# Kernel optimization log

Measured on AMD Instinct MI355X. Metric: run time of the kernel, lower is better.

The kernel has to match this reference:

```python
import jax, jax.numpy as jnp
import numpy as np

N = 50000      # nodes
E = 800000     # edges (avg degree 16)
F0 = 3         # node feature dim
EF = 3         # edge feature dim
C = 4          # num classes


def _lin_params(k, din, dout):
    k1, k2 = jax.random.split(k)
    s = 1.0 / np.sqrt(din)
    W = jax.random.uniform(k1, (dout, din), jnp.float32, -s, s)
    b = jax.random.uniform(k2, (dout,), jnp.float32, -s, s)
    return W, b


def setup_inputs() -> dict:
    key = jax.random.key(0)
    ks = jax.random.split(key, 8)
    x = jax.random.normal(ks[0], (N, F0), jnp.float32)
    edge_index = jax.random.randint(ks[1], (2, E), 0, N, jnp.int32)
    edge_attr = jax.random.uniform(ks[2], (E, EF), dtype=jnp.float32)
    W1, b1 = _lin_params(ks[3], 2 * F0 + EF, 128)
    W2, b2 = _lin_params(ks[4], 2 * 128 + EF, 64)
    W3, b3 = _lin_params(ks[5], 2 * 64 + EF, 32)
    Wc, bc = _lin_params(ks[6], 32, C)
    return dict(x=x, edge_index=edge_index, edge_attr=edge_attr,
                W1=W1, b1=b1, W2=W2, b2=b2, W3=W3, b3=b3, Wc=Wc, bc=bc)


def _edgeconv(x, src, dst, ea, W, b, n):
    # message = Linear(cat([x_i, x_j, edge_attr])); aggregated by scatter-add to dst (x_i side).
    # Split W so the node-side matmuls happen once per node instead of per edge.
    f = x.shape[1]
    Wi, Wj, We = W[:, :f], W[:, f:2 * f], W[:, 2 * f:]
    ai = x @ Wi.T   # [N, out]
    aj = x @ Wj.T   # [N, out]
    msg = ai[dst] + aj[src] + ea @ We.T + b  # [E_aug, out]
    return jax.ops.segment_sum(msg, dst, num_segments=n)


def reference(x, edge_index, edge_attr, W1, b1, W2, b2, W3, b3, Wc, bc):
    n = x.shape[0]
    loops = jnp.arange(n, dtype=edge_index.dtype)
    src = jnp.concatenate([edge_index[0], loops])  # x_j indices
    dst = jnp.concatenate([edge_index[1], loops])  # x_i indices (aggregation targets)
    ea = jnp.concatenate([edge_attr, jnp.zeros((n, edge_attr.shape[1]), edge_attr.dtype)])
    h = jax.nn.relu(_edgeconv(x, src, dst, ea, W1, b1, n))
    h = jax.nn.relu(_edgeconv(h, src, dst, ea, W2, b2, n))
    h = _edgeconv(h, src, dst, ea, W3, b3, n)  # no relu after conv3 in the original
    logits = h @ Wc.T + bc
    return jax.nn.log_softmax(logits, axis=1)
```

## Files before the change

kernel.cpp:

```cpp
#include <hip/hip_runtime.h>
#include <math.h>


static inline size_t align256(size_t x) { return (x + 255) & ~size_t(255); }

typedef unsigned short ushort_t;
using frag8  = __attribute__((ext_vector_type(8))) short;
using f32x4v = __attribute__((ext_vector_type(4))) float;
using half8  = __attribute__((ext_vector_type(8))) _Float16;

__device__ inline unsigned short f2bf(float f) {
    unsigned u = __float_as_uint(f);
    unsigned r = (u + 0x7fffu + ((u >> 16) & 1u)) >> 16;
    return (unsigned short)r;
}
__device__ inline float bflo(unsigned u) { return __uint_as_float(u << 16); }
__device__ inline float bfhi(unsigned u) { return __uint_as_float(u & 0xffff0000u); }
__device__ inline ushort_t f2hbits(float f) {
    _Float16 h = (_Float16)f;
    ushort_t u;
    __builtin_memcpy(&u, &h, 2);
    return u;
}


__global__ __launch_bounds__(256) void prep(
    const int* __restrict__ ei, int* __restrict__ count,
    uint2* __restrict__ csrp, const float* __restrict__ ea, int E,
    const float* __restrict__ x, float4* __restrict__ xpad, int n,
    const float* __restrict__ W2, ushort_t* __restrict__ W2bf,
    const float* __restrict__ W3, const float* __restrict__ b3,
    const float* __restrict__ Wc, const float* __restrict__ bc,
    float* __restrict__ AB, float* __restrict__ consts,
    int eb4, int nxb)
{
    const int t = threadIdx.x;
    const int b = blockIdx.x;
    if (b < eb4) {
        int e4 = (b * 256 + t) * 4;
        if (e4 >= E) return;
        if (e4 + 3 < E) {
            int4 s = *(const int4*)(ei + e4);
            int4 d = *(const int4*)(ei + E + e4);
            float4 a = *(const float4*)(ea + (size_t)e4 * 3);
            float4 bq = *(const float4*)(ea + (size_t)e4 * 3 + 4);
            float4 c = *(const float4*)(ea + (size_t)e4 * 3 + 8);
            int4 po;
            po.x = atomicAdd(&count[d.x], 1);
            po.y = atomicAdd(&count[d.y], 1);
            po.z = atomicAdd(&count[d.z], 1);
            po.w = atomicAdd(&count[d.w], 1);
            float ev[12] = { a.x, a.y, a.z, a.w, bq.x, bq.y, bq.z, bq.w, c.x, c.y, c.z, c.w };
            int sv[4] = { s.x, s.y, s.z, s.w };
            int dv[4] = { d.x, d.y, d.z, d.w };
            int pv[4] = { po.x, po.y, po.z, po.w };
            #pragma unroll
            for (int r = 0; r < 4; ++r) {
                uint2 p;
                p.x = (unsigned)f2bf(ev[r * 3 + 0]) | ((unsigned)f2bf(ev[r * 3 + 1]) << 16);
                p.y = (unsigned)f2bf(ev[r * 3 + 2]) | ((unsigned)sv[r] << 16);
                if (pv[r] < 64)
                    csrp[((size_t)dv[r] << 6) + pv[r]] = p;
            }
        } else {
            for (int e = e4; e < E; ++e) {
                int sv = ei[e], dv = ei[E + e];
                int po = atomicAdd(&count[dv], 1);
                uint2 p;
                p.x = (unsigned)f2bf(ea[e * 3 + 0]) | ((unsigned)f2bf(ea[e * 3 + 1]) << 16);
                p.y = (unsigned)f2bf(ea[e * 3 + 2]) | ((unsigned)sv << 16);
                if (po < 64)
                    csrp[((size_t)dv << 6) + po] = p;
            }
        }
    } else if (b < eb4 + nxb) {
        int j = (b - eb4) * 256 + t;
        if (j < n) {
            const float* xp = x + (size_t)j * 3;
            xpad[j] = make_float4(xp[0], xp[1], xp[2], 0.f);
        }
    } else if (b < eb4 + nxb + 4) {
        int wb = b - (eb4 + nxb);
        int i0 = wb * 4096 + t;
        int i1 = (wb + 1) * 4096;
        for (int idx = i0; idx < i1; idx += 256) {
            int jg = idx >> 7, k = idx & 127;
            float w = (jg < 64) ? W2[jg * 259 + k] : W2[(jg - 64) * 259 + 128 + k];
            W2bf[idx] = f2bf(w);
        }
    } else {
        for (int idx = t; idx < 512; idx += 256) {
            int j = idx >> 6, k = idx & 63;
            int jj = j & 3;
            int base = (j >= 4) ? 64 : 0;
            float s = 0.f;
            #pragma unroll
            for (int c = 0; c < 32; ++c)
                s += Wc[jj * 32 + c] * W3[c * 131 + base + k];
            AB[idx] = s;
        }
        if (t < 4) {
            float db = 0.f;
            for (int c = 0; c < 32; ++c) db += Wc[t * 32 + c] * b3[c];
            consts[t] = db;
            consts[4 + t] = bc[t];
            for (int q = 0; q < 3; ++q) {
                float s = 0.f;
                for (int c = 0; c < 32; ++c) s += Wc[t * 32 + c] * W3[c * 131 + 128 + q];
                consts[8 + t * 3 + q] = s;
            }
        }
    }
}


__global__ __launch_bounds__(256) void h1_gemm(
    const float4* __restrict__ xpad, const float* __restrict__ W1,
    const float* __restrict__ b1, const float* __restrict__ b2,
    const int* __restrict__ count,
    const uint2* __restrict__ csrp, float4* __restrict__ eagg4,
    const ushort_t* __restrict__ W2bf,
    _Float16* __restrict__ AI2, _Float16* __restrict__ AJ2, int n_nodes)
{
    constexpr int HS = 152;
    constexpr int OS = 72;
    __shared__ float sM[10 * 128];
    __shared__ ushort_t sH[64 * HS];

    const int tid = threadIdx.x;
    for (int t = tid; t < 1280; t += 256) {
        int k = t >> 7, c = t & 127;
        int cp = (c & 31) * 4 + (c >> 5);
        sM[k * 128 + cp] = (k < 9) ? W1[c * 9 + k] : b1[c];
    }
    __syncthreads();

    const int base = blockIdx.x * 64;

    {
        const int nl = tid >> 2, ch4 = tid & 3;
        const int n = base + nl;
        if (n < n_nodes) {
            int s0 = n << 6;
            int s1 = s0 + count[n];
            float xx = 0.f, xy = 0.f, xz = 0.f, ex = 0.f, ey = 0.f, ez = 0.f;
            int i = s0 + ch4;
            for (; i + 12 < s1; i += 16) {
                uint2 p0 = csrp[i];
                uint2 p1 = csrp[i + 4];
                uint2 p2 = csrp[i + 8];
                uint2 p3 = csrp[i + 12];
                float4 xv0 = xpad[(int)(p0.y >> 16)];
                float4 xv1 = xpad[(int)(p1.y >> 16)];
                float4 xv2 = xpad[(int)(p2.y >> 16)];
                float4 xv3 = xpad[(int)(p3.y >> 16)];
                ex += (bflo(p0.x) + bflo(p1.x)) + (bflo(p2.x) + bflo(p3.x));
                ey += (bfhi(p0.x) + bfhi(p1.x)) + (bfhi(p2.x) + bfhi(p3.x));
                ez += (bflo(p0.y) + bflo(p1.y)) + (bflo(p2.y) + bflo(p3.y));
                xx += (xv0.x + xv1.x) + (xv2.x + xv3.x);
                xy += (xv0.y + xv1.y) + (xv2.y + xv3.y);
                xz += (xv0.z + xv1.z) + (xv2.z + xv3.z);
            }
            for (; i < s1; i += 4) {
                uint2 p0 = csrp[i];
                float4 xv0 = xpad[(int)(p0.y >> 16)];
                ex += bflo(p0.x); ey += bfhi(p0.x); ez += bflo(p0.y);
                xx += xv0.x; xy += xv0.y; xz += xv0.z;
            }
            #pragma unroll
            for (int off = 1; off < 4; off <<= 1) {
                xx += __shfl_xor(xx, off); xy += __shfl_xor(xy, off); xz += __shfl_xor(xz, off);
                ex += __shfl_xor(ex, off); ey += __shfl_xor(ey, off); ez += __shfl_xor(ez, off);
            }
            float deg = (float)(count[n] + 1);
            float4 xs = xpad[n];
            float v[10] = { deg * xs.x, deg * xs.y, deg * xs.z,
                            xs.x + xx, xs.y + xy, xs.z + xz,
                            ex, ey, ez, deg };
            #pragma unroll
            for (int h = 0; h < 2; ++h) {
                float hv[16];
                #pragma unroll
                for (int q = 0; q < 16; ++q) {
                    int cq = h * 16 + q;
                    float s = 0.f;
                    #pragma unroll
                    for (int k = 0; k < 10; ++k) s += v[k] * sM[k * 128 + cq * 4 + ch4];
                    hv[q] = fmaxf(s, 0.f);
                }
                uint4 u0, u1;
                u0.x = (unsigned)f2bf(hv[0]) | ((unsigned)f2bf(hv[1]) << 16);
                u0.y = (unsigned)f2bf(hv[2]) | ((unsigned)f2bf(hv[3]) << 16);
                u0.z = (unsigned)f2bf(hv[4]) | ((unsigned)f2bf(hv[5]) << 16);
                u0.w = (unsigned)f2bf(hv[6]) | ((unsigned)f2bf(hv[7]) << 16);
                u1.x = (unsigned)f2bf(hv[8]) | ((unsigned)f2bf(hv[9]) << 16);
                u1.y = (unsigned)f2bf(hv[10]) | ((unsigned)f2bf(hv[11]) << 16);
                u1.z = (unsigned)f2bf(hv[12]) | ((unsigned)f2bf(hv[13]) << 16);
                u1.w = (unsigned)f2bf(hv[14]) | ((unsigned)f2bf(hv[15]) << 16);
                *(uint4*)(sH + nl * HS + ch4 * 32 + h * 16) = u0;
                *(uint4*)(sH + nl * HS + ch4 * 32 + h * 16 + 8) = u1;
            }
            if (ch4 == 0) eagg4[n] = make_float4(ex, ey, ez, 0.f);
        } else {
            *(uint4*)(sH + nl * HS + ch4 * 32) = make_uint4(0, 0, 0, 0);
            *(uint4*)(sH + nl * HS + ch4 * 32 + 8) = make_uint4(0, 0, 0, 0);
            *(uint4*)(sH + nl * HS + ch4 * 32 + 16) = make_uint4(0, 0, 0, 0);
            *(uint4*)(sH + nl * HS + ch4 * 32 + 24) = make_uint4(0, 0, 0, 0);
        }
    }
    __syncthreads();

    const int wave = tid >> 6, wl = tid & 63;
    const int m = wl & 15, quad = wl >> 4;

    frag8 a[4];
    #pragma unroll
    for (int ks = 0; ks < 4; ++ks)
        a[ks] = *(const frag8*)(sH + (wave * 16 + m) * HS + ks * 32 + quad * 8);

    f32x4v acc[8];
    #pragma unroll
    for (int t = 0; t < 8; ++t) acc[t] = (f32x4v)(0.f);

    #pragma unroll
    for (int t = 0; t < 8; ++t) {
        #pragma unroll
        for (int ks = 0; ks < 4; ++ks) {
            frag8 b = *(const frag8*)(W2bf + (t * 16 + m) * 128 + ks * 32 + quad * 8);
            acc[t] = __builtin_amdgcn_mfma_f32_16x16x32_bf16(a[ks], b, acc[t], 0, 0, 0);
        }
    }

    float b2v[4];
    #pragma unroll
    for (int t = 0; t < 4; ++t) b2v[t] = b2[t * 16 + m];

    __syncthreads();
    ushort_t* sAI = sH;
    ushort_t* sAJ = sH + 64 * OS;

    #pragma unroll
    for (int reg = 0; reg < 4; ++reg) {
        int rl = wave * 16 + quad * 4 + reg;
        #pragma unroll
        for (int t = 0; t < 4; ++t)
            sAI[rl * OS + t * 16 + m] = f2hbits(acc[t][reg] + b2v[t]);
        #pragma unroll
        for (int t = 4; t < 8; ++t)
            sAJ[rl * OS + (t - 4) * 16 + m] = f2hbits(acc[t][reg]);
    }
    __syncthreads();

    for (int idx = tid; idx < 512; idx += 256) {
        int row = idx >> 3, seg = idx & 7;
        int grow = base + row;
        if (grow < n_nodes) {
            *(uint4*)((ushort_t*)AI2 + (size_t)grow * 64 + seg * 8) =
                *(const uint4*)(sAI + row * OS + seg * 8);
            *(uint4*)((ushort_t*)AJ2 + (size_t)grow * 64 + seg * 8) =
                *(const uint4*)(sAJ + row * OS + seg * 8);
        }
    }
}


__global__ __launch_bounds__(256) void gather2(
    const _Float16* __restrict__ AI2, const _Float16* __restrict__ AJ2,
    const float* __restrict__ W2, const int* __restrict__ count,
    const float4* __restrict__ eagg4,
    const uint2* __restrict__ csrp, const float* __restrict__ AB,
    float* __restrict__ U, float* __restrict__ Z, int n_nodes)
{
    __shared__ float sAB[512];
    __shared__ float sWe[192];
    const int tid = threadIdx.x;
    for (int t = tid; t < 512; t += 256) sAB[t] = AB[t];
    for (int t = tid; t < 192; t += 256) {
        int c = t / 3, q = t % 3;
        sWe[t] = W2[c * 259 + 256 + q];
    }
    __syncthreads();

    int wl = tid & 63;
    int grp = wl >> 3, ch8 = wl & 7;
    int n = blockIdx.x * 32 + (tid >> 6) * 8 + grp;
    if (n >= n_nodes) return;

    int s0 = n << 6;
    int s1 = s0 + count[n];

    half8 hacc0 = (half8)(_Float16)0.f;
    half8 hacc1 = (half8)(_Float16)0.f;
    int base = s0;
    for (; base + 8 < s1; base += 16) {
        int jA = base + ch8;
        int jB = base + 8 + ch8; if (jB >= s1) jB = s1 - 1;
        int myA = (int)(csrp[jA].y >> 16);
        int myB = (int)(csrp[jB].y >> 16);
        int cntB = s1 - (base + 8); if (cntB > 8) cntB = 8;
        #pragma unroll
        for (int k = 0; k < 8; ++k) {
            int s = __shfl(myA, grp * 8 + k);
            half8 v = *(const half8*)(AJ2 + (size_t)s * 64 + ch8 * 8);
            if (k & 1) hacc1 += v; else hacc0 += v;
        }
        #pragma unroll
        for (int k = 0; k < 8; ++k) {
            int s = __shfl(myB, grp * 8 + k);
            if (k < cntB) {
                half8 v = *(const half8*)(AJ2 + (size_t)s * 64 + ch8 * 8);
                if (k & 1) hacc1 += v; else hacc0 += v;
            }
        }
    }
    if (base < s1) {
        int j = base + ch8; if (j >= s1) j = s1 - 1;
        int my = (int)(csrp[j].y >> 16);
        int cnt = s1 - base; if (cnt > 8) cnt = 8;
        #pragma unroll
        for (int k = 0; k < 8; ++k) {
            int s = __shfl(my, grp * 8 + k);
            if (k < cnt) {
                half8 v = *(const half8*)(AJ2 + (size_t)s * 64 + ch8 * 8);
                if (k & 1) hacc1 += v; else hacc0 += v;
            }
        }
    }
    float acc[8];
    #pragma unroll
    for (int q = 0; q < 8; ++q) acc[q] = (float)hacc0[q] + (float)hacc1[q];

    float deg = (float)(s1 - s0 + 1);
    float4 e4 = eagg4[n];
    half8 ai = *(const half8*)(AI2 + (size_t)n * 64 + ch8 * 8);
    half8 su = *(const half8*)(AJ2 + (size_t)n * 64 + ch8 * 8);
    float r[8];
    #pragma unroll
    for (int q = 0; q < 8; ++q) {
        int c = ch8 * 8 + q;
        float we = sWe[c * 3] * e4.x + sWe[c * 3 + 1] * e4.y + sWe[c * 3 + 2] * e4.z;
        r[q] = fmaxf(deg * (float)ai[q] + (float)su[q] + we + acc[q], 0.f);
    }
    float pj[8];
    #pragma unroll
    for (int j = 0; j < 8; ++j) {
        float4 wA = *(const float4*)(sAB + j * 64 + ch8 * 8);
        float4 wB = *(const float4*)(sAB + j * 64 + ch8 * 8 + 4);
        pj[j] = r[0] * wA.x + r[1] * wA.y + r[2] * wA.z + r[3] * wA.w
              + r[4] * wB.x + r[5] * wB.y + r[6] * wB.z + r[7] * wB.w;
    }
    #pragma unroll
    for (int off = 1; off < 8; off <<= 1)
        #pragma unroll
        for (int j = 0; j < 8; ++j) pj[j] += __shfl_xor(pj[j], off);

    if (ch8 == 0) {
        *(float4*)(U + (size_t)n * 4) = make_float4(pj[0], pj[1], pj[2], pj[3]);
        *(float4*)(Z + (size_t)n * 4) = make_float4(pj[4], pj[5], pj[6], pj[7]);
    }
}


__global__ __launch_bounds__(256) void final_softmax(
    const float* __restrict__ U, const float* __restrict__ Z,
    const int* __restrict__ count, const float4* __restrict__ eagg4,
    const uint2* __restrict__ csrp, const float* __restrict__ consts,
    float* __restrict__ out, int n_nodes)
{
    int wl = threadIdx.x & 63;
    int grp = wl >> 3, ch8 = wl & 7;
    int n = blockIdx.x * 32 + (threadIdx.x >> 6) * 8 + grp;
    if (n >= n_nodes) return;

    int s0 = n << 6;
    int s1 = s0 + count[n];
    float ax = 0.f, ay = 0.f, az = 0.f, aw = 0.f;
    int i = s0 + ch8;
    for (; i + 8 < s1; i += 16) {
        int sA = (int)(csrp[i].y >> 16);
        int sB = (int)(csrp[i + 8].y >> 16);
        float4 zA = *(const float4*)(Z + (size_t)sA * 4);
        float4 zB = *(const float4*)(Z + (size_t)sB * 4);
        ax += zA.x + zB.x; ay += zA.y + zB.y;
        az += zA.z + zB.z; aw += zA.w + zB.w;
    }
    if (i < s1) {
        int sA = (int)(csrp[i].y >> 16);
        float4 zA = *(const float4*)(Z + (size_t)sA * 4);
        ax += zA.x; ay += zA.y; az += zA.z; aw += zA.w;
    }
    #pragma unroll
    for (int off = 1; off < 8; off <<= 1) {
        ax += __shfl_xor(ax, off); ay += __shfl_xor(ay, off);
        az += __shfl_xor(az, off); aw += __shfl_xor(aw, off);
    }
    if (ch8 != 0) return;

    float deg = (float)(s1 - s0 + 1);
    float4 u = *(const float4*)(U + (size_t)n * 4);
    float4 zs = *(const float4*)(Z + (size_t)n * 4);
    float4 e4 = eagg4[n];
    float av[4] = { ax + zs.x, ay + zs.y, az + zs.z, aw + zs.w };
    float uv[4] = { u.x, u.y, u.z, u.w };
    float lg[4];
    #pragma unroll
    for (int j = 0; j < 4; ++j) {
        lg[j] = deg * (uv[j] + consts[j]) + av[j] + consts[4 + j]
              + consts[8 + j * 3] * e4.x + consts[9 + j * 3] * e4.y
              + consts[10 + j * 3] * e4.z;
    }
    float m = fmaxf(fmaxf(lg[0], lg[1]), fmaxf(lg[2], lg[3]));
    float lse = logf(expf(lg[0] - m) + expf(lg[1] - m) + expf(lg[2] - m) + expf(lg[3] - m));
    *(float4*)(out + (size_t)n * 4) =
        make_float4(lg[0] - m - lse, lg[1] - m - lse, lg[2] - m - lse, lg[3] - m - lse);
}


extern "C" void kernel_launch(void* const* d_in, const int* in_sizes, int n_in,
                              void* d_out, int out_size, void* d_ws, size_t ws_size,
                              hipStream_t stream)
{
    const float* x    = (const float*)d_in[0];
    const int*   ei   = (const int*)  d_in[1];
    const float* ea   = (const float*)d_in[2];
    const float* W1   = (const float*)d_in[3];
    const float* b1   = (const float*)d_in[4];
    const float* W2   = (const float*)d_in[5];
    const float* b2   = (const float*)d_in[6];
    const float* W3   = (const float*)d_in[7];
    const float* b3   = (const float*)d_in[8];
    const float* Wc   = (const float*)d_in[9];
    const float* bc   = (const float*)d_in[10];
    float* out = (float*)d_out;

    const int N = in_sizes[0] / 3;
    const int E = in_sizes[1] / 2;

    char* ws = (char*)d_ws;
    size_t off = 0;
    int*    count    = (int*)(ws + off);            off = align256(off + (size_t)N * 4);
    uint2*  csrp     = (uint2*)(ws + off);          off = align256(off + (size_t)N * 64 * 8);
    float*  AB       = (float*)(ws + off);          off = align256(off + 512 * 4);
    float*  consts   = (float*)(ws + off);          off = align256(off + 32 * 4);
    ushort_t* W2bf   = (ushort_t*)(ws + off);       off = align256(off + 128 * 128 * 2);
    float4* xpad     = (float4*)(ws + off);         off = align256(off + (size_t)N * 16);
    float4* eagg4    = (float4*)(ws + off);         off = align256(off + (size_t)N * 16);
    _Float16* AI2    = (_Float16*)(ws + off);       off = align256(off + (size_t)N * 64 * 2);
    _Float16* AJ2    = (_Float16*)(ws + off);       off = align256(off + (size_t)N * 64 * 2);
    float*  Ubuf     = (float*)(ws + off);          off = align256(off + (size_t)N * 16);
    float*  Zbuf     = (float*)(ws + off);          off = align256(off + (size_t)N * 16);
    (void)ws_size;

    hipMemsetAsync(count, 0, (size_t)N * 4, stream);

    const int eb4 = ((E + 3) / 4 + 255) / 256;
    const int nxb = (N + 255) / 256;

    prep<<<eb4 + nxb + 5, 256, 0, stream>>>(ei, count, csrp, ea, E,
                                            x, xpad, N, W2, W2bf,
                                            W3, b3, Wc, bc, AB, consts,
                                            eb4, nxb);

    h1_gemm<<<(N + 63) / 64, 256, 0, stream>>>(xpad, W1, b1, b2, count, csrp,
                                               eagg4, W2bf, AI2, AJ2, N);

    const int gb = (N + 31) / 32;
    gather2<<<gb, 256, 0, stream>>>(AI2, AJ2, W2, count, eagg4, csrp, AB, Ubuf, Zbuf, N);

    final_softmax<<<gb, 256, 0, stream>>>(Ubuf, Zbuf, count, eagg4, csrp, consts, out, N);
}
```

Before: 191.1 us.

## Partition edge bucketing into eight destination ranges for scatter locality

The CSR-building phase of prep now launches eight times as many edge blocks. Each block handles one of eight contiguous destination-node ranges and only processes edges whose destination falls in that range. The intent is to localize the atomicAdd counters and csrp writes into a smaller working set that fits in cache. In exchange, every destination index is read eight times, and src and edge attributes are loaded with scalar, uncoalesced reads.

After: 180.2 us (median of 2 runs). 5.7% less time.

```diff
diff --git a/kernel.cpp b/kernel.cpp
--- a/kernel.cpp
+++ b/kernel.cpp
@@ -32,55 +32,49 @@
     const float* __restrict__ W3, const float* __restrict__ b3,
     const float* __restrict__ Wc, const float* __restrict__ bc,
     float* __restrict__ AB, float* __restrict__ consts,
-    int eb4, int nxb)
+    int eb8, int nxb, int rs)
 {
     const int t = threadIdx.x;
     const int b = blockIdx.x;
-    if (b < eb4) {
-        int e4 = (b * 256 + t) * 4;
+    if (b < eb8) {
+        const int c = b & 7;
+        const int j = b >> 3;
+        const int lo = c * rs;
+        const int hi = (lo + rs < n) ? lo + rs : n;
+        int e4 = (j * 256 + t) * 4;
         if (e4 >= E) return;
+        int4 d;
         if (e4 + 3 < E) {
-            int4 s = *(const int4*)(ei + e4);
-            int4 d = *(const int4*)(ei + E + e4);
-            float4 a = *(const float4*)(ea + (size_t)e4 * 3);
-            float4 bq = *(const float4*)(ea + (size_t)e4 * 3 + 4);
-            float4 c = *(const float4*)(ea + (size_t)e4 * 3 + 8);
-            int4 po;
-            po.x = atomicAdd(&count[d.x], 1);
-            po.y = atomicAdd(&count[d.y], 1);
-            po.z = atomicAdd(&count[d.z], 1);
-            po.w = atomicAdd(&count[d.w], 1);
-            float ev[12] = { a.x, a.y, a.z, a.w, bq.x, bq.y, bq.z, bq.w, c.x, c.y, c.z, c.w };
-            int sv[4] = { s.x, s.y, s.z, s.w };
-            int dv[4] = { d.x, d.y, d.z, d.w };
-            int pv[4] = { po.x, po.y, po.z, po.w };
-            #pragma unroll
-            for (int r = 0; r < 4; ++r) {
+            d = *(const int4*)(ei + E + e4);
+        } else {
+            d.x = ei[E + e4];
+            d.y = (e4 + 1 < E) ? ei[E + e4 + 1] : -1;
+            d.z = (e4 + 2 < E) ? ei[E + e4 + 2] : -1;
+            d.w = (e4 + 3 < E) ? ei[E + e4 + 3] : -1;
+        }
+        int dv[4] = { d.x, d.y, d.z, d.w };
+        #pragma unroll
+        for (int r = 0; r < 4; ++r) {
+            if (dv[r] >= lo && dv[r] < hi) {
+                int e = e4 + r;
+                int sv = ei[e];
+                int po = atomicAdd(&count[dv[r]], 1);
                 uint2 p;
-                p.x = (unsigned)f2bf(ev[r * 3 + 0]) | ((unsigned)f2bf(ev[r * 3 + 1]) << 16);
-                p.y = (unsigned)f2bf(ev[r * 3 + 2]) | ((unsigned)sv[r] << 16);
-                if (pv[r] < 64)
-                    csrp[((size_t)dv[r] << 6) + pv[r]] = p;
-            }
-        } else {
-            for (int e = e4; e < E; ++e) {
-                int sv = ei[e], dv = ei[E + e];
-                int po = atomicAdd(&count[dv], 1);
-                uint2 p;
-                p.x = (unsigned)f2bf(ea[e * 3 + 0]) | ((unsigned)f2bf(ea[e * 3 + 1]) << 16);
-                p.y = (unsigned)f2bf(ea[e * 3 + 2]) | ((unsigned)sv << 16);
+                p.x = (unsigned)f2bf(ea[(size_t)e * 3 + 0])
+                    | ((unsigned)f2bf(ea[(size_t)e * 3 + 1]) << 16);
+                p.y = (unsigned)f2bf(ea[(size_t)e * 3 + 2]) | ((unsigned)sv << 16);
                 if (po < 64)
-                    csrp[((size_t)dv << 6) + po] = p;
-            }
-        }
-    } else if (b < eb4 + nxb) {
-        int j = (b - eb4) * 256 + t;
+                    csrp[((size_t)dv[r] << 6) + po] = p;
+            }
+        }
+    } else if (b < eb8 + nxb) {
+        int j = (b - eb8) * 256 + t;
         if (j < n) {
             const float* xp = x + (size_t)j * 3;
             xpad[j] = make_float4(xp[0], xp[1], xp[2], 0.f);
         }
-    } else if (b < eb4 + nxb + 4) {
-        int wb = b - (eb4 + nxb);
+    } else if (b < eb8 + nxb + 4) {
+        int wb = b - (eb8 + nxb);
         int i0 = wb * 4096 + t;
         int i1 = (wb + 1) * 4096;
         for (int idx = i0; idx < i1; idx += 256) {
@@ -454,12 +448,14 @@
     hipMemsetAsync(count, 0, (size_t)N * 4, stream);
 
     const int eb4 = ((E + 3) / 4 + 255) / 256;
+    const int eb8 = eb4 * 8;
     const int nxb = (N + 255) / 256;
-
-    prep<<<eb4 + nxb + 5, 256, 0, stream>>>(ei, count, csrp, ea, E,
+    const int rs  = (N + 7) / 8;
+
+    prep<<<eb8 + nxb + 5, 256, 0, stream>>>(ei, count, csrp, ea, E,
                                             x, xpad, N, W2, W2bf,
                                             W3, b3, Wc, bc, AB, consts,
-                                            eb4, nxb);
+                                            eb8, nxb, rs);
 
     h1_gemm<<<(N + 63) / 64, 256, 0, stream>>>(xpad, W1, b1, b2, count, csrp,
                                                eagg4, W2bf, AI2, AJ2, N);
```
